# Kernel tuning notes

Hardware: AMD Instinct MI355X
Metric: run time of the kernel (lower is better)

## Reference

```python
import jax, jax.numpy as jnp
import numpy as np

CLIP_MAX = 1.0 / 1e-06  # torch.clip(1/d, max=1/1e-6)


def setup_inputs() -> dict:
    key = jax.random.key(0)
    k1, k2 = jax.random.split(key)
    base_features = jax.random.normal(k1, (4096, 512), dtype=jnp.float32)
    target_features = jax.random.normal(k2, (8192, 512), dtype=jnp.float32)
    return {"base_features": base_features, "target_features": target_features}


def _pairwise_euclidean(x, y):
    # Same math as sqrt(sum((x[:,None,:]-y[None,:,:])**2, -1)) but computed
    # via the expanded form to avoid materializing the (N,M,D) intermediate.
    x2 = jnp.sum(x * x, axis=1, keepdims=True)          # [N,1]
    y2 = jnp.sum(y * y, axis=1, keepdims=True).T        # [1,M]
    xy = x @ y.T                                        # [N,M]
    sq = jnp.maximum(x2 + y2 - 2.0 * xy, 0.0)
    return jnp.sqrt(sq)


def reference(base_features, target_features):
    # distance == 'euclidean' branch of SimilarityCalculatorFeatureOnly.forward
    dist = _pairwise_euclidean(base_features, target_features)   # [N,M]
    similarity = jnp.minimum(1.0 / dist, CLIP_MAX)                # clip at 1e6
    return (base_features, similarity)
```

## Files before the change

### kernel.cpp

```cpp
#include <hip/hip_runtime.h>
#include <hip/hip_bf16.h>
#include <stdint.h>

typedef short bf16x8 __attribute__((ext_vector_type(8)));
typedef float f32x4 __attribute__((ext_vector_type(4)));

#define D  512
#define NB 4096
#define NT 8192

__device__ __forceinline__ unsigned short f2bf(float f) {
    __hip_bfloat16 h = __float2bfloat16(f);
    return *reinterpret_cast<unsigned short*>(&h);
}

__global__ __launch_bounds__(256) void prep_kernel(
    const float* __restrict__ x, const float* __restrict__ y,
    unsigned short* __restrict__ xb, unsigned short* __restrict__ yb,
    float* __restrict__ x2, float* __restrict__ y2, float* __restrict__ copy)
{
    const int grow = blockIdx.x * 4 + (threadIdx.x >> 6);
    const int lane = threadIdx.x & 63;
    const bool isX = grow < NB;
    const int row  = isX ? grow : grow - NB;
    const float* src = isX ? x : y;
    unsigned short* dst = isX ? xb : yb;
    float* norms = isX ? x2 : y2;

    const float4* rp = reinterpret_cast<const float4*>(src + (size_t)row * D);
    float4 v0 = rp[lane * 2];
    float4 v1 = rp[lane * 2 + 1];
    if (isX) {
        float4* cp = reinterpret_cast<float4*>(copy + (size_t)row * D);
        cp[lane * 2]     = v0;
        cp[lane * 2 + 1] = v1;
    }
    float s = v0.x*v0.x + v0.y*v0.y + v0.z*v0.z + v0.w*v0.w
            + v1.x*v1.x + v1.y*v1.y + v1.z*v1.z + v1.w*v1.w;
    union { unsigned short h[8]; int4 v; } u;
    u.h[0] = f2bf(v0.x); u.h[1] = f2bf(v0.y); u.h[2] = f2bf(v0.z); u.h[3] = f2bf(v0.w);
    u.h[4] = f2bf(v1.x); u.h[5] = f2bf(v1.y); u.h[6] = f2bf(v1.z); u.h[7] = f2bf(v1.w);
    reinterpret_cast<int4*>(dst + (size_t)row * D)[lane] = u.v;
    #pragma unroll
    for (int off = 32; off > 0; off >>= 1) s += __shfl_xor(s, off);
    if (lane == 0) norms[row] = s;
}

__global__ __launch_bounds__(256, 2) void gemm_sim_kernel(
    const unsigned short* __restrict__ X, const unsigned short* __restrict__ Y,
    const float* __restrict__ x2, const float* __restrict__ y2,
    float* __restrict__ out)
{
    __shared__ alignas(16) unsigned short lds[36864];

    const int t    = threadIdx.x;
    const int lane = t & 63;
    const int w    = t >> 6;

    const int bid = blockIdx.x;
    const int xcd = bid & 7;
    const int idx = bid >> 3;
    const int rowBase = ((xcd >> 2) * 16 + (idx & 15)) * 128;
    const int colBase = ((xcd & 3) * 8 + (idx >> 4)) * 256;

    const int swz = ((t & 3) ^ ((t >> 3) & 3)) * 8;
    const unsigned short* gA = X + (size_t)(rowBase + (t >> 2)) * D + swz;
    const unsigned short* gB = Y + (size_t)(colBase + (t >> 2)) * D + swz;

    const int cread = ((lane >> 4) ^ ((lane >> 1) & 3)) * 8;
    const int aoff = (lane & 15) * 32 + cread;
    const int boff = 4096 + (w * 64 + (lane & 15)) * 32 + cread;

    f32x4 acc[8][4] = {};

#define STAGE_A(BUF, KT) do { \
    _Pragma("unroll") \
    for (int L = 0; L < 2; ++L) \
        __builtin_amdgcn_global_load_lds( \
            (const __attribute__((address_space(1))) void*)(gA + (size_t)L * 64 * D + (KT) * 32), \
            (__attribute__((address_space(3))) void*)(lds + (BUF) * 12288 + t * 8 + L * 2048), 16, 0, 0); \
} while (0)

#define STAGE_B(BUF, KT) do { \
    _Pragma("unroll") \
    for (int L = 0; L < 4; ++L) \
        __builtin_amdgcn_global_load_lds( \
            (const __attribute__((address_space(1))) void*)(gB + (size_t)L * 64 * D + (KT) * 32), \
            (__attribute__((address_space(3))) void*)(lds + (BUF) * 12288 + 4096 + t * 8 + L * 2048), 16, 0, 0); \
} while (0)

    STAGE_A(0, 0); STAGE_B(0, 0);
    STAGE_A(1, 1); STAGE_B(1, 1);
    asm volatile("s_waitcnt vmcnt(6)" ::: "memory");
    __builtin_amdgcn_s_barrier();

#pragma unroll
    for (int kt = 0; kt < 16; ++kt) {
        bf16x8 _a[2][4], _b[4];
        #pragma unroll
        for (int n = 0; n < 4; ++n)
            _b[n] = *(const bf16x8*)(lds + (kt % 3) * 12288 + boff + n * 512);
        #pragma unroll
        for (int h = 0; h < 2; ++h)
            #pragma unroll
            for (int m = 0; m < 4; ++m)
                _a[h][m] = *(const bf16x8*)(lds + (kt % 3) * 12288 + aoff + h * 2048 + m * 512);
        if (kt + 2 < 16) {
            STAGE_A(((kt + 2) % 3), kt + 2);
            STAGE_B(((kt + 2) % 3), kt + 2);
        }
        __builtin_amdgcn_s_setprio(1);
        #pragma unroll
        for (int h = 0; h < 2; ++h)
            #pragma unroll
            for (int m = 0; m < 4; ++m)
                #pragma unroll
                for (int n = 0; n < 4; ++n)
                    acc[h * 4 + m][n] = __builtin_amdgcn_mfma_f32_16x16x32_bf16(
                        _a[h][m], _b[n], acc[h * 4 + m][n], 0, 0, 0);
        __builtin_amdgcn_s_setprio(0);
        __builtin_amdgcn_sched_barrier(0);
        if (kt < 14)       { asm volatile("s_waitcnt vmcnt(6)" ::: "memory"); }
        else if (kt == 14) { asm volatile("s_waitcnt vmcnt(0)" ::: "memory"); }
        if (kt < 15) __builtin_amdgcn_s_barrier();
    }
#undef STAGE_A
#undef STAGE_B

    const int col0 = colBase + w * 64 + (lane & 15);
    const int row0 = rowBase + ((lane >> 4) << 2);
    #pragma unroll
    for (int mi = 0; mi < 8; ++mi) {
        const int rbase = row0 + (mi >> 2) * 64 + (mi & 3) * 16;
        #pragma unroll
        for (int q = 0; q < 4; ++q) {
            const int grow = rbase + q;
            const float xn = x2[grow];
            float* orow = out + (size_t)grow * NT;
            #pragma unroll
            for (int n = 0; n < 4; ++n) {
                const int gcol = col0 + n * 16;
                float sq = fmaxf(xn + y2[gcol] - 2.0f * acc[mi][n][q], 0.0f);
                orow[gcol] = fminf(rsqrtf(sq), 1.0e6f);
            }
        }
    }
}

extern "C" void kernel_launch(void* const* d_in, const int* in_sizes, int n_in,
                              void* d_out, int out_size, void* d_ws, size_t ws_size,
                              hipStream_t stream)
{
    const float* x = (const float*)d_in[0];
    const float* y = (const float*)d_in[1];
    float* out = (float*)d_out;
    char* ws = (char*)d_ws;

    unsigned short* xb = (unsigned short*)ws;
    unsigned short* yb = (unsigned short*)(ws + (4u << 20));
    float* x2 = (float*)(ws + (12u << 20));
    float* y2 = (float*)(ws + (12u << 20) + 4 * NB);

    prep_kernel<<<(NB + NT) / 4, 256, 0, stream>>>(x, y, xb, yb, x2, y2, out);
    gemm_sim_kernel<<<1024, 256, 0, stream>>>(xb, yb, x2, y2, out + (size_t)NB * D);
}
```

Measured before the change: 60.60 us.

## Switch to 128x128 tiles with single-buffered K=64 stages and more occupancy

Replaces the 128x256 block tile, whose triple-buffered K=32 pipeline with async prefetch kept two blocks per CU, with a 128x128 tile using a 2x2 wave layout. The new loop uses a single LDS buffer with K=64 stages, loaded synchronously each iteration, and launches twice as many blocks with a target of three blocks per CU. The aim is to raise occupancy and hide latency across blocks instead of through in-block prefetch. In exchange it drops the overlap of loads and compute inside a block and lowers operand reuse per tile.

```diff
diff --git a/kernel.cpp b/kernel.cpp
--- a/kernel.cpp
+++ b/kernel.cpp
@@ -46,101 +46,91 @@
     if (lane == 0) norms[row] = s;
 }
 
-__global__ __launch_bounds__(256, 2) void gemm_sim_kernel(
+__global__ __launch_bounds__(256, 3) void gemm_sim_kernel(
     const unsigned short* __restrict__ X, const unsigned short* __restrict__ Y,
     const float* __restrict__ x2, const float* __restrict__ y2,
     float* __restrict__ out)
 {
-    __shared__ alignas(16) unsigned short lds[36864];
+    __shared__ alignas(16) unsigned short lds[16384];
 
     const int t    = threadIdx.x;
     const int lane = t & 63;
     const int w    = t >> 6;
+    const int wr   = w >> 1;
+    const int wc   = w & 1;
 
     const int bid = blockIdx.x;
     const int xcd = bid & 7;
     const int idx = bid >> 3;
-    const int rowBase = ((xcd >> 2) * 16 + (idx & 15)) * 128;
-    const int colBase = ((xcd & 3) * 8 + (idx >> 4)) * 256;
+    const int rowBase = ((xcd & 1) * 16 + (idx & 15)) * 128;
+    const int colBase = ((xcd >> 1) * 16 + (idx >> 4)) * 128;
 
-    const int swz = ((t & 3) ^ ((t >> 3) & 3)) * 8;
-    const unsigned short* gA = X + (size_t)(rowBase + (t >> 2)) * D + swz;
-    const unsigned short* gB = Y + (size_t)(colBase + (t >> 2)) * D + swz;
+    const int g = ((t & 7) ^ ((t >> 3) & 7)) * 8;
+    const unsigned short* gA = X + (size_t)(rowBase + (t >> 3)) * D + g;
+    const unsigned short* gB = Y + (size_t)(colBase + (t >> 3)) * D + g;
 
-    const int cread = ((lane >> 4) ^ ((lane >> 1) & 3)) * 8;
-    const int aoff = (lane & 15) * 32 + cread;
-    const int boff = 4096 + (w * 64 + (lane & 15)) * 32 + cread;
+    int sc[2];
+    #pragma unroll
+    for (int kk = 0; kk < 2; ++kk)
+        sc[kk] = (((kk << 2) | (lane >> 4)) ^ (lane & 7)) * 8;
+    const int arow = (wr * 64 + (lane & 15)) * 64;
+    const int brow = 8192 + (wc * 64 + (lane & 15)) * 64;
 
-    f32x4 acc[8][4] = {};
+    f32x4 acc[4][4] = {};
 
-#define STAGE_A(BUF, KT) do { \
+#define STAGE(KT) do { \
     _Pragma("unroll") \
-    for (int L = 0; L < 2; ++L) \
+    for (int L = 0; L < 4; ++L) { \
         __builtin_amdgcn_global_load_lds( \
-            (const __attribute__((address_space(1))) void*)(gA + (size_t)L * 64 * D + (KT) * 32), \
-            (__attribute__((address_space(3))) void*)(lds + (BUF) * 12288 + t * 8 + L * 2048), 16, 0, 0); \
+            (const __attribute__((address_space(1))) void*)(gA + (size_t)L * 32 * D + (KT) * 64), \
+            (__attribute__((address_space(3))) void*)(lds + t * 8 + L * 2048), 16, 0, 0); \
+        __builtin_amdgcn_global_load_lds( \
+            (const __attribute__((address_space(1))) void*)(gB + (size_t)L * 32 * D + (KT) * 64), \
+            (__attribute__((address_space(3))) void*)(lds + 8192 + t * 8 + L * 2048), 16, 0, 0); \
+    } \
 } while (0)
 
-#define STAGE_B(BUF, KT) do { \
-    _Pragma("unroll") \
-    for (int L = 0; L < 4; ++L) \
-        __builtin_amdgcn_global_load_lds( \
-            (const __attribute__((address_space(1))) void*)(gB + (size_t)L * 64 * D + (KT) * 32), \
-            (__attribute__((address_space(3))) void*)(lds + (BUF) * 12288 + 4096 + t * 8 + L * 2048), 16, 0, 0); \
-} while (0)
-
-    STAGE_A(0, 0); STAGE_B(0, 0);
-    STAGE_A(1, 1); STAGE_B(1, 1);
-    asm volatile("s_waitcnt vmcnt(6)" ::: "memory");
-    __builtin_amdgcn_s_barrier();
-
 #pragma unroll
-    for (int kt = 0; kt < 16; ++kt) {
-        bf16x8 _a[2][4], _b[4];
+    for (int kt = 0; kt < 8; ++kt) {
+        STAGE(kt);
+        asm volatile("s_waitcnt vmcnt(0)" ::: "memory");
+        __builtin_amdgcn_s_barrier();
         #pragma unroll
-        for (int n = 0; n < 4; ++n)
-            _b[n] = *(const bf16x8*)(lds + (kt % 3) * 12288 + boff + n * 512);
-        #pragma unroll
-        for (int h = 0; h < 2; ++h)
+        for (int kk = 0; kk < 2; ++kk) {
+            bf16x8 a[4], b[4];
             #pragma unroll
             for (int m = 0; m < 4; ++m)
-                _a[h][m] = *(const bf16x8*)(lds + (kt % 3) * 12288 + aoff + h * 2048 + m * 512);
-        if (kt + 2 < 16) {
-            STAGE_A(((kt + 2) % 3), kt + 2);
-            STAGE_B(((kt + 2) % 3), kt + 2);
-        }
-        __builtin_amdgcn_s_setprio(1);
-        #pragma unroll
-        for (int h = 0; h < 2; ++h)
+                a[m] = *(const bf16x8*)(lds + arow + m * 1024 + sc[kk]);
+            #pragma unroll
+            for (int n = 0; n < 4; ++n)
+                b[n] = *(const bf16x8*)(lds + brow + n * 1024 + sc[kk]);
+            __builtin_amdgcn_s_setprio(1);
             #pragma unroll
             for (int m = 0; m < 4; ++m)
                 #pragma unroll
                 for (int n = 0; n < 4; ++n)
-                    acc[h * 4 + m][n] = __builtin_amdgcn_mfma_f32_16x16x32_bf16(
-                        _a[h][m], _b[n], acc[h * 4 + m][n], 0, 0, 0);
-        __builtin_amdgcn_s_setprio(0);
-        __builtin_amdgcn_sched_barrier(0);
-        if (kt < 14)       { asm volatile("s_waitcnt vmcnt(6)" ::: "memory"); }
-        else if (kt == 14) { asm volatile("s_waitcnt vmcnt(0)" ::: "memory"); }
-        if (kt < 15) __builtin_amdgcn_s_barrier();
+                    acc[m][n] = __builtin_amdgcn_mfma_f32_16x16x32_bf16(
+                        a[m], b[n], acc[m][n], 0, 0, 0);
+            __builtin_amdgcn_s_setprio(0);
+        }
+        asm volatile("s_waitcnt lgkmcnt(0)" ::: "memory");
+        if (kt < 7) __builtin_amdgcn_s_barrier();
     }
-#undef STAGE_A
-#undef STAGE_B
+#undef STAGE
 
-    const int col0 = colBase + w * 64 + (lane & 15);
-    const int row0 = rowBase + ((lane >> 4) << 2);
+    const int col0 = colBase + wc * 64 + (lane & 15);
+    const int row0 = rowBase + wr * 64 + ((lane >> 4) << 2);
     #pragma unroll
-    for (int mi = 0; mi < 8; ++mi) {
-        const int rbase = row0 + (mi >> 2) * 64 + (mi & 3) * 16;
+    for (int m = 0; m < 4; ++m) {
         #pragma unroll
         for (int q = 0; q < 4; ++q) {
-            const int grow = rbase + q;
+            const int grow = row0 + m * 16 + q;
             const float xn = x2[grow];
             float* orow = out + (size_t)grow * NT;
             #pragma unroll
             for (int n = 0; n < 4; ++n) {
                 const int gcol = col0 + n * 16;
-                float sq = fmaxf(xn + y2[gcol] - 2.0f * acc[mi][n][q], 0.0f);
+                float sq = fmaxf(xn + y2[gcol] - 2.0f * acc[m][n][q], 0.0f);
                 orow[gcol] = fminf(rsqrtf(sq), 1.0e6f);
             }
         }
@@ -162,5 +152,5 @@
     float* y2 = (float*)(ws + (12u << 20) + 4 * NB);
 
     prep_kernel<<<(NB + NT) / 4, 256, 0, stream>>>(x, y, xb, yb, x2, y2, out);
-    gemm_sim_kernel<<<1024, 256, 0, stream>>>(xb, yb, x2, y2, out + (size_t)NB * D);
+    gemm_sim_kernel<<<2048, 256, 0, stream>>>(xb, yb, x2, y2, out + (size_t)NB * D);
 }
```

Result: faster. 59.02 us (-2.6%).
